# Kernel tuning notes

Hardware: AMD Instinct MI355X
Metric: run time of the kernel (lower is better)

The kernel has to match this reference:

```python
import jax, jax.numpy as jnp
import numpy as np

D_MODEL = 768
HEADS = 12
D_K = D_MODEL // HEADS
NEG = -1e9


def setup_inputs() -> dict:
    key = jax.random.key(0)
    ks = jax.random.split(key, 7)
    B, S, D = 4, 2048, D_MODEL
    scale = 1.0 / np.sqrt(D)
    q = jax.random.normal(ks[0], (B, S, D), dtype=jnp.float32)
    k = jax.random.normal(ks[1], (B, S, D), dtype=jnp.float32)
    v = jax.random.normal(ks[2], (B, S, D), dtype=jnp.float32)
    # causal mask, broadcastable over batch and heads; mask==0 -> -1e9
    mask = jnp.tril(jnp.ones((1, 1, S, S), dtype=jnp.int32))
    W_q = jax.random.normal(ks[3], (D, D), dtype=jnp.float32) * scale
    W_k = jax.random.normal(ks[4], (D, D), dtype=jnp.float32) * scale
    W_v = jax.random.normal(ks[5], (D, D), dtype=jnp.float32) * scale
    W_o = jax.random.normal(ks[6], (D, D), dtype=jnp.float32) * scale
    return {"q": q, "k": k, "v": v, "mask": mask,
            "W_q": W_q, "W_k": W_k, "W_v": W_v, "W_o": W_o}


def reference(q, k, v, mask, W_q, W_k, W_v, W_o):
    B, S, D = q.shape
    # nn.Linear(bias=False): y = x @ W.T
    query = (q @ W_q.T).reshape(B, S, HEADS, D_K).transpose(0, 2, 1, 3)  # [B,H,S,dk]
    key_ = (k @ W_k.T).reshape(B, S, HEADS, D_K).transpose(0, 2, 1, 3)
    value = (v @ W_v.T).reshape(B, S, HEADS, D_K).transpose(0, 2, 1, 3)
    scores = jnp.einsum('bhqd,bhkd->bhqk', query, key_) / jnp.sqrt(
        jnp.asarray(D_K, dtype=query.dtype))
    scores = jnp.where(mask == 0, jnp.asarray(NEG, dtype=scores.dtype), scores)
    attn = jax.nn.softmax(scores, axis=-1)
    # dropout rate = 0.0 (inference / eval mode): identity
    x = jnp.einsum('bhqk,bhkd->bhqd', attn, value)  # [B,H,S,dk]
    x = x.transpose(0, 2, 1, 3).reshape(B, S, D)
    return x @ W_o.T
```

## Files before the change

kernel.cpp:

```cpp
#include <hip/hip_runtime.h>


typedef _Float16 f16x8 __attribute__((ext_vector_type(8)));
typedef _Float16 f16x4 __attribute__((ext_vector_type(4)));
typedef float floatx4 __attribute__((ext_vector_type(4)));
typedef float floatx16 __attribute__((ext_vector_type(16)));

#define MFMA16(a, b, c) __builtin_amdgcn_mfma_f32_16x16x32_f16((a), (b), (c), 0, 0, 0)
#define MFMA32(a, b, c) __builtin_amdgcn_mfma_f32_32x32x16_f16((a), (b), (c), 0, 0, 0)

static constexpr int B_ = 4;
static constexpr int S_ = 2048;
static constexpr int D_ = 768;
static constexpr int H_ = 12;
static constexpr int DK = 64;

__device__ __forceinline__ f16x8 cvt8(float4 a, float4 b) {
  f16x8 h;
  h[0] = (_Float16)a.x; h[1] = (_Float16)a.y;
  h[2] = (_Float16)a.z; h[3] = (_Float16)a.w;
  h[4] = (_Float16)b.x; h[5] = (_Float16)b.y;
  h[6] = (_Float16)b.z; h[7] = (_Float16)b.w;
  return h;
}

__device__ __forceinline__ void dma16(const _Float16* g, _Float16* l) {
  __builtin_amdgcn_global_load_lds(
      (const __attribute__((address_space(1))) unsigned int*)g,
      (__attribute__((address_space(3))) unsigned int*)l, 16, 0, 0);
}

struct CvtArgs {
  const float* src[7];
  _Float16* dst[7];
  int end[7];
  int nseg;
};

__global__ __launch_bounds__(256) void cvt_f32_f16(CvtArgs a) {
  int b = blockIdx.x;
  int s = 0;
  while (s < a.nseg - 1 && b >= a.end[s]) ++s;
  int local = b - (s ? a.end[s - 1] : 0);
  const int tid = threadIdx.x;
  const float4* p = (const float4*)(a.src[s] + (size_t)local * 2048) + tid * 2;
  float4 x0 = p[0], x1 = p[1];
  *(f16x8*)(a.dst[s] + (size_t)local * 2048 + tid * 8) = cvt8(x0, x1);
}

static constexpr int PAN = 128 * 32;

struct QkvPtrs {
  const void* a[3];
  const void* w[3];
};

template <int MODE, bool SCALE>
__device__ __forceinline__ void gemm_core64(const _Float16* __restrict__ A,
                                            const _Float16* __restrict__ Bm,
                                            void* __restrict__ Cv,
                                            _Float16* As, _Float16* Bs,
                                            int m0, int n0, int N, int K) {
  const int tid = threadIdx.x;
  const int wave = tid >> 6, lane = tid & 63;
  const int l15 = lane & 15, quad = lane >> 4;
  const int wm = (wave >> 1) * 64, wn = (wave & 1) * 64;
  const int lr = lane >> 2;
  const int lc = (lane & 3) * 8;
  const int wb = wave * 16;

  floatx4 acc[4][4] = {};

  for (int k0 = 0; k0 < K; k0 += 64) {
    {
      const _Float16* g = A + (size_t)(m0 + wb + lr) * K + k0 + lc;
      dma16(g, As + wb * 32);
      dma16(g + 32, As + PAN + wb * 32);
      const _Float16* g2 = g + (size_t)64 * K;
      dma16(g2, As + (64 + wb) * 32);
      dma16(g2 + 32, As + PAN + (64 + wb) * 32);
    }
    {
      const _Float16* g = Bm + (size_t)(n0 + wb + lr) * K + k0 + lc;
      dma16(g, Bs + wb * 32);
      dma16(g + 32, Bs + PAN + wb * 32);
      const _Float16* g2 = g + (size_t)64 * K;
      dma16(g2, Bs + (64 + wb) * 32);
      dma16(g2 + 32, Bs + PAN + (64 + wb) * 32);
    }
    __syncthreads();

#pragma unroll
    for (int p = 0; p < 2; ++p) {
      f16x8 af[4], bf[4];
#pragma unroll
      for (int t = 0; t < 4; ++t)
        af[t] = *(const f16x8*)(As + p * PAN + (wm + t * 16 + l15) * 32 +
                                quad * 8);
#pragma unroll
      for (int t = 0; t < 4; ++t)
        bf[t] = *(const f16x8*)(Bs + p * PAN + (wn + t * 16 + l15) * 32 +
                                quad * 8);
#pragma unroll
      for (int mt = 0; mt < 4; ++mt)
#pragma unroll
        for (int nt = 0; nt < 4; ++nt)
          acc[mt][nt] = MFMA16(af[mt], bf[nt], acc[mt][nt]);
    }
    __syncthreads();
  }

  if constexpr (MODE == 2) {
#pragma unroll
    for (int mt = 0; mt < 4; ++mt)
#pragma unroll
      for (int nt = 0; nt < 4; ++nt) {
        int row = m0 + wm + mt * 16 + quad * 4;
        int col = n0 + wn + nt * 16 + l15;
        int b = row >> 11, s = row & 2047;
        int h = col >> 6, d = col & 63;
        f16x4 v4;
#pragma unroll
        for (int r = 0; r < 4; ++r) v4[r] = (_Float16)acc[mt][nt][r];
        *(f16x4*)((_Float16*)Cv + ((size_t)(b * H_ + h) * DK + d) * S_ + s) =
            v4;
      }
  } else {
#pragma unroll
    for (int mt = 0; mt < 4; ++mt)
#pragma unroll
      for (int nt = 0; nt < 4; ++nt)
#pragma unroll
        for (int r = 0; r < 4; ++r) {
          int row = m0 + wm + mt * 16 + quad * 4 + r;
          int col = n0 + wn + nt * 16 + l15;
          float val = acc[mt][nt][r];
          if constexpr (SCALE) val *= 0.125f;
          if constexpr (MODE == 0) {
            ((float*)Cv)[(size_t)row * N + col] = val;
          } else {
            int b = row >> 11, s = row & 2047;
            int h = col >> 6, d = col & 63;
            ((_Float16*)Cv)[((size_t)(b * H_ + h) * S_ + s) * DK + d] =
                (_Float16)val;
          }
        }
  }
}

__global__ __launch_bounds__(256) void qkv_gemm64(QkvPtrs P, _Float16* Qh,
                                                  _Float16* Kh, _Float16* Vt) {
  __shared__ _Float16 As[2 * PAN];
  __shared__ _Float16 Bs[2 * PAN];
  const int linear =
      blockIdx.x + gridDim.x * (blockIdx.y + gridDim.y * blockIdx.z);
  const int xcd = linear & 7;
  const int idx = linear >> 3;
  const int z = idx / 48;
  const int r = idx % 48;
  const int mp = xcd * 8 + (r / 6);
  const int n = r % 6;
  const int m0 = mp * 128, n0 = n * 128;
  if (z == 0) {
    gemm_core64<1, true>((const _Float16*)P.a[0], (const _Float16*)P.w[0], Qh,
                         As, Bs, m0, n0, D_, D_);
  } else if (z == 1) {
    gemm_core64<1, false>((const _Float16*)P.a[1], (const _Float16*)P.w[1], Kh,
                          As, Bs, m0, n0, D_, D_);
  } else {
    gemm_core64<2, false>((const _Float16*)P.a[2], (const _Float16*)P.w[2], Vt,
                          As, Bs, m0, n0, D_, D_);
  }
}

static constexpr int PAN_A = 64 * 32;
static constexpr int PAN_B = 128 * 32;

__global__ __launch_bounds__(256) void gemm_o64(const _Float16* __restrict__ A,
                                                const _Float16* __restrict__ W,
                                                float* __restrict__ C) {
  __shared__ _Float16 As[2 * PAN_A];
  __shared__ _Float16 Bs[2 * PAN_B];
  constexpr int K = 768, N = 768;

  const int linear = blockIdx.x + gridDim.x * blockIdx.y;
  const int xcd = linear & 7;
  const int idx = linear >> 3;
  const int mp = xcd * 16 + idx / 6;
  const int n = idx % 6;
  const int m0 = mp * 64, n0 = n * 128;

  const int tid = threadIdx.x;
  const int wave = tid >> 6, lane = tid & 63;
  const int l15 = lane & 15, quad = lane >> 4;
  const int wm = (wave >> 1) * 32, wn = (wave & 1) * 64;
  const int lr = lane >> 2, lc = (lane & 3) * 8;

  floatx4 acc[2][4] = {};

  for (int k0 = 0; k0 < K; k0 += 64) {
#pragma unroll
    for (int p = 0; p < 2; ++p) {
      const _Float16* g =
          A + (size_t)(m0 + wave * 16 + lr) * K + k0 + p * 32 + lc;
      dma16(g, As + p * PAN_A + wave * 16 * 32);
    }
#pragma unroll
    for (int p = 0; p < 2; ++p)
#pragma unroll
      for (int q = 0; q < 2; ++q) {
        const _Float16* g =
            W + (size_t)(n0 + wave * 32 + q * 16 + lr) * K + k0 + p * 32 + lc;
        dma16(g, Bs + p * PAN_B + (wave * 32 + q * 16) * 32);
      }
    __syncthreads();

#pragma unroll
    for (int p = 0; p < 2; ++p) {
      f16x8 af[2], bf[4];
#pragma unroll
      for (int t = 0; t < 2; ++t)
        af[t] = *(const f16x8*)(As + p * PAN_A + (wm + t * 16 + l15) * 32 +
                                quad * 8);
#pragma unroll
      for (int t = 0; t < 4; ++t)
        bf[t] = *(const f16x8*)(Bs + p * PAN_B + (wn + t * 16 + l15) * 32 +
                                quad * 8);
#pragma unroll
      for (int mt = 0; mt < 2; ++mt)
#pragma unroll
        for (int nt = 0; nt < 4; ++nt)
          acc[mt][nt] = MFMA16(af[mt], bf[nt], acc[mt][nt]);
    }
    __syncthreads();
  }

#pragma unroll
  for (int mt = 0; mt < 2; ++mt)
#pragma unroll
    for (int nt = 0; nt < 4; ++nt)
#pragma unroll
      for (int r = 0; r < 4; ++r) {
        int row = m0 + wm + mt * 16 + quad * 4 + r;
        int col = n0 + wn + nt * 16 + l15;
        C[(size_t)row * N + col] = acc[mt][nt][r];
      }
}

__global__ __launch_bounds__(256, 3) void flash_attn(
    const _Float16* __restrict__ Qh, const _Float16* __restrict__ Kh,
    const _Float16* __restrict__ Vt, _Float16* __restrict__ Oh) {
  __shared__ _Float16 Ks[128 * 72];
  __shared__ _Float16 Vts[64 * 136];
  __shared__ _Float16 Ps[4][32 * 36];

  const int tid = threadIdx.x;
  const int wave = tid >> 6, lane = tid & 63;
  const int l31 = lane & 31, sub = lane >> 5;
  const int rowhalf = wave & 1, keyhalf = wave >> 1;

  const int linear = blockIdx.x + gridDim.x * blockIdx.y;
  const int xcd = linear & 7;
  const int seq = linear >> 3;
  const int bh = xcd * 6 + (seq >> 4);
  const int xp = seq & 15;
  const int b = bh / H_, h = bh % H_;
  const size_t base = (size_t)bh * S_ * DK;
  const size_t basev = (size_t)bh * DK * S_;

  const int srow = tid >> 2;
  const int scol = (tid & 3) * 16;
  const int vcol = (tid & 3) * 32;

  for (int c = 0; c < 2; ++c) {
    const int qt = c ? xp : 31 - xp;
    const int q0 = qt * 64;
    const int nt = qt + 1;
    const int iters = (nt + 1) >> 1;
    const int rbase = q0 + rowhalf * 32;

    f16x8 qf[4];
#pragma unroll
    for (int ks = 0; ks < 4; ++ks)
      qf[ks] = *(const f16x8*)(Qh + base + (size_t)(rbase + l31) * DK +
                               ks * 16 + sub * 8);

    floatx16 o0 = {}, o1 = {};
    float plsum[16] = {};

    f16x8 pk[4], pv[4];
    {
      const _Float16* kp = Kh + base + (size_t)srow * DK + scol;
      pk[0] = *(const f16x8*)kp;
      pk[1] = *(const f16x8*)(kp + 8);
      const _Float16* kp2 = kp + (size_t)64 * DK;
      pk[2] = *(const f16x8*)kp2;
      pk[3] = *(const f16x8*)(kp2 + 8);
      const _Float16* vp = Vt + basev + (size_t)srow * S_ + vcol;
#pragma unroll
      for (int j = 0; j < 4; ++j) pv[j] = *(const f16x8*)(vp + j * 8);
    }

    for (int i = 0; i < iters; ++i) {
      __syncthreads();
      *(f16x8*)(Ks + srow * 72 + scol) = pk[0];
      *(f16x8*)(Ks + srow * 72 + scol + 8) = pk[1];
      *(f16x8*)(Ks + (64 + srow) * 72 + scol) = pk[2];
      *(f16x8*)(Ks + (64 + srow) * 72 + scol + 8) = pk[3];
#pragma unroll
      for (int j = 0; j < 4; ++j)
        *(f16x8*)(Vts + srow * 136 + vcol + j * 8) = pv[j];
      __syncthreads();

      if (i + 1 < iters) {
        const int g0 = (i + 1) * 128;
        const _Float16* kp = Kh + base + (size_t)(g0 + srow) * DK + scol;
        pk[0] = *(const f16x8*)kp;
        pk[1] = *(const f16x8*)(kp + 8);
        const _Float16* kp2 = kp + (size_t)64 * DK;
        pk[2] = *(const f16x8*)kp2;
        pk[3] = *(const f16x8*)(kp2 + 8);
        const _Float16* vp = Vt + basev + (size_t)srow * S_ + g0 + vcol;
#pragma unroll
        for (int j = 0; j < 4; ++j) pv[j] = *(const f16x8*)(vp + j * 8);
      }

      const int kb = i * 128 + keyhalf * 64;
      if (kb > rbase + 31) continue;

      floatx16 s0 = {}, s1 = {};
#pragma unroll
      for (int ks = 0; ks < 4; ++ks) {
        f16x8 kf0 = *(const f16x8*)(Ks + (keyhalf * 64 + l31) * 72 + ks * 16 +
                                    sub * 8);
        f16x8 kf1 = *(const f16x8*)(Ks + (keyhalf * 64 + 32 + l31) * 72 +
                                    ks * 16 + sub * 8);
        s0 = MFMA32(qf[ks], kf0, s0);
        s1 = MFMA32(qf[ks], kf1, s1);
      }

#pragma unroll
      for (int t = 0; t < 2; ++t) {
        floatx16 sv = t ? s1 : s0;
        const int cg = kb + t * 32 + l31;
        const bool nm = (kb + t * 32 + 31 > rbase);
#pragma unroll
        for (int reg = 0; reg < 16; ++reg) {
          float s = sv[reg];
          if (nm) {
            int rg = rbase + (reg & 3) + 8 * (reg >> 2) + 4 * sub;
            if (cg > rg) s = -1e30f;
          }
          float e = __expf(s);
          plsum[reg] += e;
          Ps[wave][((reg & 3) + 8 * (reg >> 2) + 4 * sub) * 36 + l31] =
              (_Float16)e;
        }
        f16x8 pf0 = *(const f16x8*)(Ps[wave] + l31 * 36 + sub * 8);
        f16x8 pf1 = *(const f16x8*)(Ps[wave] + l31 * 36 + 16 + sub * 8);
        const int kk = keyhalf * 64 + t * 32;
        f16x8 va0 = *(const f16x8*)(Vts + l31 * 136 + kk + sub * 8);
        f16x8 va1 = *(const f16x8*)(Vts + l31 * 136 + kk + 16 + sub * 8);
        f16x8 vb0 = *(const f16x8*)(Vts + (32 + l31) * 136 + kk + sub * 8);
        f16x8 vb1 = *(const f16x8*)(Vts + (32 + l31) * 136 + kk + 16 + sub * 8);
        o0 = MFMA32(pf0, va0, o0);
        o0 = MFMA32(pf1, va1, o0);
        o1 = MFMA32(pf0, vb0, o1);
        o1 = MFMA32(pf1, vb1, o1);
      }
    }

#pragma unroll
    for (int reg = 0; reg < 16; ++reg) {
      float l = plsum[reg];
      l += __shfl_xor(l, 1);
      l += __shfl_xor(l, 2);
      l += __shfl_xor(l, 4);
      l += __shfl_xor(l, 8);
      l += __shfl_xor(l, 16);
      plsum[reg] = l;
    }

    float* fb = (float*)Ks;
    float* lb = (float*)Vts;
    __syncthreads();
    if (keyhalf == 1) {
      float* d0 = fb + rowhalf * 2048 + lane * 32;
#pragma unroll
      for (int reg = 0; reg < 16; ++reg) {
        d0[reg] = o0[reg];
        d0[16 + reg] = o1[reg];
      }
      float* dl = lb + rowhalf * 1024 + lane * 16;
#pragma unroll
      for (int reg = 0; reg < 16; ++reg) dl[reg] = plsum[reg];
    }
    __syncthreads();
    if (keyhalf == 0) {
      const float* s0p = fb + rowhalf * 2048 + lane * 32;
      const float* slp = lb + rowhalf * 1024 + lane * 16;
#pragma unroll
      for (int reg = 0; reg < 16; ++reg) {
        float inv = 1.0f / (plsum[reg] + slp[reg]);
        int row = rbase + (reg & 3) + 8 * (reg >> 2) + 4 * sub;
        float v0 = (o0[reg] + s0p[reg]) * inv;
        float v1 = (o1[reg] + s0p[16 + reg]) * inv;
        _Float16* op = Oh + ((size_t)(b * S_ + row)) * D_ + h * DK;
        op[l31] = (_Float16)v0;
        op[32 + l31] = (_Float16)v1;
      }
    }
    __syncthreads();
  }
}

template <int MODE, bool SCALE>
__global__ __launch_bounds__(256) void gemm128(const float* __restrict__ Av,
                                               const float* __restrict__ Bv,
                                               void* __restrict__ Cv, int M,
                                               int N, int K) {
  __shared__ _Float16 As[128 * 40];
  __shared__ _Float16 Bs[128 * 40];

  const int tid = threadIdx.x;
  const int wave = tid >> 6, lane = tid & 63;
  const int l15 = lane & 15, quad = lane >> 4;
  const int wm = (wave >> 1) * 64, wn = (wave & 1) * 64;
  const int m0 = blockIdx.y * 128, n0 = blockIdx.x * 128;
  const int srow = tid >> 1, scol = (tid & 1) * 16;

  floatx4 acc[4][4] = {};

  for (int k0 = 0; k0 < K; k0 += 32) {
    {
      const float4* p =
          (const float4*)(Av + (size_t)(m0 + srow) * K + k0 + scol);
      float4 x0 = p[0], x1 = p[1], x2 = p[2], x3 = p[3];
      *(f16x8*)(As + srow * 40 + scol) = cvt8(x0, x1);
      *(f16x8*)(As + srow * 40 + scol + 8) = cvt8(x2, x3);
    }
    {
      const float4* p =
          (const float4*)(Bv + (size_t)(n0 + srow) * K + k0 + scol);
      float4 x0 = p[0], x1 = p[1], x2 = p[2], x3 = p[3];
      *(f16x8*)(Bs + srow * 40 + scol) = cvt8(x0, x1);
      *(f16x8*)(Bs + srow * 40 + scol + 8) = cvt8(x2, x3);
    }
    __syncthreads();

    f16x8 af[4], bf[4];
#pragma unroll
    for (int t = 0; t < 4; ++t)
      af[t] = *(const f16x8*)(As + (wm + t * 16 + l15) * 40 + quad * 8);
#pragma unroll
    for (int t = 0; t < 4; ++t)
      bf[t] = *(const f16x8*)(Bs + (wn + t * 16 + l15) * 40 + quad * 8);
#pragma unroll
    for (int mt = 0; mt < 4; ++mt)
#pragma unroll
      for (int nt = 0; nt < 4; ++nt)
        acc[mt][nt] = MFMA16(af[mt], bf[nt], acc[mt][nt]);
    __syncthreads();
  }

#pragma unroll
  for (int mt = 0; mt < 4; ++mt)
#pragma unroll
    for (int nt = 0; nt < 4; ++nt)
#pragma unroll
      for (int r = 0; r < 4; ++r) {
        int row = m0 + wm + mt * 16 + quad * 4 + r;
        int col = n0 + wn + nt * 16 + l15;
        float val = acc[mt][nt][r];
        if constexpr (SCALE) val *= 0.125f;
        if constexpr (MODE == 0) {
          ((float*)Cv)[(size_t)row * N + col] = val;
        } else if constexpr (MODE == 1) {
          int b = row >> 11, s = row & 2047;
          int h = col >> 6, d = col & 63;
          ((_Float16*)Cv)[((size_t)(b * H_ + h) * S_ + s) * DK + d] =
              (_Float16)val;
        } else {
          int b = col >> 11, s = col & 2047;
          int h = row >> 6, d = row & 63;
          ((_Float16*)Cv)[((size_t)(b * H_ + h) * DK + d) * S_ + s] =
              (_Float16)val;
        }
      }
}

__global__ __launch_bounds__(256) void gemm_out_f32w(
    const _Float16* __restrict__ A, const float* __restrict__ Bv,
    float* __restrict__ C) {
  __shared__ _Float16 As[128 * 40];
  __shared__ _Float16 Bs[128 * 40];
  constexpr int K = 768, N = 768;

  const int tid = threadIdx.x;
  const int wave = tid >> 6, lane = tid & 63;
  const int l15 = lane & 15, quad = lane >> 4;
  const int wm = (wave >> 1) * 64, wn = (wave & 1) * 64;
  const int m0 = blockIdx.y * 128, n0 = blockIdx.x * 128;
  const int srow = tid >> 1, scol = (tid & 1) * 16;

  floatx4 acc[4][4] = {};

  for (int k0 = 0; k0 < K; k0 += 32) {
    {
      const f16x8* p = (const f16x8*)(A + (size_t)(m0 + srow) * K + k0 + scol);
      *(f16x8*)(As + srow * 40 + scol) = p[0];
      *(f16x8*)(As + srow * 40 + scol + 8) = p[1];
    }
    {
      const float4* p =
          (const float4*)(Bv + (size_t)(n0 + srow) * K + k0 + scol);
      float4 x0 = p[0], x1 = p[1], x2 = p[2], x3 = p[3];
      *(f16x8*)(Bs + srow * 40 + scol) = cvt8(x0, x1);
      *(f16x8*)(Bs + srow * 40 + scol + 8) = cvt8(x2, x3);
    }
    __syncthreads();

    f16x8 af[4], bf[4];
#pragma unroll
    for (int t = 0; t < 4; ++t)
      af[t] = *(const f16x8*)(As + (wm + t * 16 + l15) * 40 + quad * 8);
#pragma unroll
    for (int t = 0; t < 4; ++t)
      bf[t] = *(const f16x8*)(Bs + (wn + t * 16 + l15) * 40 + quad * 8);
#pragma unroll
    for (int mt = 0; mt < 4; ++mt)
#pragma unroll
      for (int nt = 0; nt < 4; ++nt)
        acc[mt][nt] = MFMA16(af[mt], bf[nt], acc[mt][nt]);
    __syncthreads();
  }

#pragma unroll
  for (int mt = 0; mt < 4; ++mt)
#pragma unroll
    for (int nt = 0; nt < 4; ++nt)
#pragma unroll
      for (int r = 0; r < 4; ++r) {
        int row = m0 + wm + mt * 16 + quad * 4 + r;
        int col = n0 + wn + nt * 16 + l15;
        C[(size_t)row * N + col] = acc[mt][nt][r];
      }
}

extern "C" void kernel_launch(void* const* d_in, const int* in_sizes, int n_in,
                              void* d_out, int out_size, void* d_ws,
                              size_t ws_size, hipStream_t stream) {
  const float* q = (const float*)d_in[0];
  const float* k = (const float*)d_in[1];
  const float* v = (const float*)d_in[2];
  const float* Wq = (const float*)d_in[4];
  const float* Wk = (const float*)d_in[5];
  const float* Wv = (const float*)d_in[6];
  const float* Wo = (const float*)d_in[7];
  float* out = (float*)d_out;

  const size_t E = (size_t)B_ * H_ * S_ * DK;
  const size_t EW = (size_t)D_ * D_;
  _Float16* Qh = (_Float16*)d_ws;
  _Float16* Kh = Qh + E;
  _Float16* Vt = Kh + E;
  _Float16* Oh = Vt + E;

  const int M = B_ * S_;
  dim3 blk(256);
  dim3 qg(D_ / 128, M / 128, 3);
  dim3 og(D_ / 128, M / 64);
  dim3 pg(D_ / 128, M / 128);
  dim3 fg(16, B_ * H_);

  const size_t need_full = (7 * E + 4 * EW) * 2;

  if (ws_size >= need_full) {
    _Float16* qf = Oh + E;
    _Float16* kf = qf + E;
    _Float16* vf = kf + E;
    _Float16* wqf = vf + E;
    _Float16* wkf = wqf + EW;
    _Float16* wvf = wkf + EW;
    _Float16* wof = wvf + EW;
    CvtArgs ca;
    ca.src[0] = q;  ca.dst[0] = qf;
    ca.src[1] = k;  ca.dst[1] = kf;
    ca.src[2] = v;  ca.dst[2] = vf;
    ca.src[3] = Wq; ca.dst[3] = wqf;
    ca.src[4] = Wk; ca.dst[4] = wkf;
    ca.src[5] = Wv; ca.dst[5] = wvf;
    ca.src[6] = Wo; ca.dst[6] = wof;
    int ends[7] = {3072, 6144, 9216, 9504, 9792, 10080, 10368};
    for (int i = 0; i < 7; ++i) ca.end[i] = ends[i];
    ca.nseg = 7;
    cvt_f32_f16<<<10368, blk, 0, stream>>>(ca);
    QkvPtrs P;
    P.a[0] = qf; P.a[1] = kf; P.a[2] = vf;
    P.w[0] = wqf; P.w[1] = wkf; P.w[2] = wvf;
    qkv_gemm64<<<qg, blk, 0, stream>>>(P, Qh, Kh, Vt);
    flash_attn<<<fg, blk, 0, stream>>>(Qh, Kh, Vt, Oh);
    gemm_o64<<<og, blk, 0, stream>>>(Oh, wof, out);
  } else {
    gemm128<1, true><<<pg, blk, 0, stream>>>(q, Wq, Qh, M, D_, D_);
    gemm128<1, false><<<pg, blk, 0, stream>>>(k, Wk, Kh, M, D_, D_);
    gemm128<2, false><<<dim3(M / 128, D_ / 128), blk, 0, stream>>>(
        Wv, v, Vt, D_, M, D_);
    flash_attn<<<fg, blk, 0, stream>>>(Qh, Kh, Vt, Oh);
    gemm_out_f32w<<<pg, blk, 0, stream>>>(Oh, Wo, out);
  }
}
```

Measured before the change: 299.7 us.

## Load K/V tiles into LDS via direct global-to-LDS DMA instead of register staging

Replaces the register-prefetched K and V tile loads, previously written to padded LDS, with direct global-to-LDS DMA copies (dma16) into an unpadded, panel-split layout of 32-element rows. The point is to free the VGPRs used for prefetch staging and skip the register round trip through ds_write. In exchange, the software prefetch of the next tile is gone: each iteration now issues loads and waits at the barrier, with no overlap of memory and compute. The unpadded 32-wide rows may also cause LDS bank conflicts on the MFMA operand reads.

After: 274.2 us. -8.5%, faster.

```diff
diff --git a/kernel.cpp b/kernel.cpp
--- a/kernel.cpp
+++ b/kernel.cpp
@@ -250,14 +250,16 @@
 __global__ __launch_bounds__(256, 3) void flash_attn(
     const _Float16* __restrict__ Qh, const _Float16* __restrict__ Kh,
     const _Float16* __restrict__ Vt, _Float16* __restrict__ Oh) {
-  __shared__ _Float16 Ks[128 * 72];
-  __shared__ _Float16 Vts[64 * 136];
+  __shared__ _Float16 Ks[2 * 128 * 32];
+  __shared__ _Float16 Vts[4 * 64 * 32];
   __shared__ _Float16 Ps[4][32 * 36];
 
   const int tid = threadIdx.x;
   const int wave = tid >> 6, lane = tid & 63;
   const int l31 = lane & 31, sub = lane >> 5;
   const int rowhalf = wave & 1, keyhalf = wave >> 1;
+  const int lr = lane >> 2;
+  const int lc = (lane & 3) * 8;
 
   const int linear = blockIdx.x + gridDim.x * blockIdx.y;
   const int xcd = linear & 7;
@@ -268,15 +270,10 @@
   const size_t base = (size_t)bh * S_ * DK;
   const size_t basev = (size_t)bh * DK * S_;
 
-  const int srow = tid >> 2;
-  const int scol = (tid & 3) * 16;
-  const int vcol = (tid & 3) * 32;
-
   for (int c = 0; c < 2; ++c) {
     const int qt = c ? xp : 31 - xp;
     const int q0 = qt * 64;
-    const int nt = qt + 1;
-    const int iters = (nt + 1) >> 1;
+    const int iters = (qt + 2) >> 1;
     const int rbase = q0 + rowhalf * 32;
 
     f16x8 qf[4];
@@ -288,86 +285,74 @@
     floatx16 o0 = {}, o1 = {};
     float plsum[16] = {};
 
-    f16x8 pk[4], pv[4];
-    {
-      const _Float16* kp = Kh + base + (size_t)srow * DK + scol;
-      pk[0] = *(const f16x8*)kp;
-      pk[1] = *(const f16x8*)(kp + 8);
-      const _Float16* kp2 = kp + (size_t)64 * DK;
-      pk[2] = *(const f16x8*)kp2;
-      pk[3] = *(const f16x8*)(kp2 + 8);
-      const _Float16* vp = Vt + basev + (size_t)srow * S_ + vcol;
-#pragma unroll
-      for (int j = 0; j < 4; ++j) pv[j] = *(const f16x8*)(vp + j * 8);
-    }
-
     for (int i = 0; i < iters; ++i) {
+      const int g0 = i * 128;
+#pragma unroll
+      for (int p = 0; p < 2; ++p)
+#pragma unroll
+        for (int qq = 0; qq < 2; ++qq) {
+          const _Float16* g = Kh + base +
+                              (size_t)(g0 + wave * 32 + qq * 16 + lr) * DK +
+                              p * 32 + lc;
+          dma16(g, Ks + p * 4096 + (wave * 32 + qq * 16) * 32);
+        }
+#pragma unroll
+      for (int p = 0; p < 4; ++p) {
+        const _Float16* g =
+            Vt + basev + (size_t)(wave * 16 + lr) * S_ + g0 + p * 32 + lc;
+        dma16(g, Vts + p * 2048 + wave * 16 * 32);
+      }
       __syncthreads();
-      *(f16x8*)(Ks + srow * 72 + scol) = pk[0];
-      *(f16x8*)(Ks + srow * 72 + scol + 8) = pk[1];
-      *(f16x8*)(Ks + (64 + srow) * 72 + scol) = pk[2];
-      *(f16x8*)(Ks + (64 + srow) * 72 + scol + 8) = pk[3];
-#pragma unroll
-      for (int j = 0; j < 4; ++j)
-        *(f16x8*)(Vts + srow * 136 + vcol + j * 8) = pv[j];
+
+      const int kb = g0 + keyhalf * 64;
+      if (kb <= rbase + 31) {
+        floatx16 s0 = {}, s1 = {};
+#pragma unroll
+        for (int ks = 0; ks < 4; ++ks) {
+          const int pp = ks >> 1;
+          const int off = (ks & 1) * 16 + sub * 8;
+          f16x8 kf0 =
+              *(const f16x8*)(Ks + pp * 4096 + (keyhalf * 64 + l31) * 32 + off);
+          f16x8 kf1 = *(const f16x8*)(Ks + pp * 4096 +
+                                      (keyhalf * 64 + 32 + l31) * 32 + off);
+          s0 = MFMA32(qf[ks], kf0, s0);
+          s1 = MFMA32(qf[ks], kf1, s1);
+        }
+
+#pragma unroll
+        for (int t = 0; t < 2; ++t) {
+          floatx16 sv = t ? s1 : s0;
+          const int cg = kb + t * 32 + l31;
+          const bool nm = (kb + t * 32 + 31 > rbase);
+#pragma unroll
+          for (int reg = 0; reg < 16; ++reg) {
+            float s = sv[reg];
+            if (nm) {
+              int rg = rbase + (reg & 3) + 8 * (reg >> 2) + 4 * sub;
+              if (cg > rg) s = -1e30f;
+            }
+            float e = __expf(s);
+            plsum[reg] += e;
+            Ps[wave][((reg & 3) + 8 * (reg >> 2) + 4 * sub) * 36 + l31] =
+                (_Float16)e;
+          }
+          f16x8 pf0 = *(const f16x8*)(Ps[wave] + l31 * 36 + sub * 8);
+          f16x8 pf1 = *(const f16x8*)(Ps[wave] + l31 * 36 + 16 + sub * 8);
+          const int vp = keyhalf * 2 + t;
+          f16x8 va0 = *(const f16x8*)(Vts + vp * 2048 + l31 * 32 + sub * 8);
+          f16x8 va1 =
+              *(const f16x8*)(Vts + vp * 2048 + l31 * 32 + 16 + sub * 8);
+          f16x8 vb0 =
+              *(const f16x8*)(Vts + vp * 2048 + (32 + l31) * 32 + sub * 8);
+          f16x8 vb1 =
+              *(const f16x8*)(Vts + vp * 2048 + (32 + l31) * 32 + 16 + sub * 8);
+          o0 = MFMA32(pf0, va0, o0);
+          o0 = MFMA32(pf1, va1, o0);
+          o1 = MFMA32(pf0, vb0, o1);
+          o1 = MFMA32(pf1, vb1, o1);
+        }
+      }
       __syncthreads();
-
-      if (i + 1 < iters) {
-        const int g0 = (i + 1) * 128;
-        const _Float16* kp = Kh + base + (size_t)(g0 + srow) * DK + scol;
-        pk[0] = *(const f16x8*)kp;
-        pk[1] = *(const f16x8*)(kp + 8);
-        const _Float16* kp2 = kp + (size_t)64 * DK;
-        pk[2] = *(const f16x8*)kp2;
-        pk[3] = *(const f16x8*)(kp2 + 8);
-        const _Float16* vp = Vt + basev + (size_t)srow * S_ + g0 + vcol;
-#pragma unroll
-        for (int j = 0; j < 4; ++j) pv[j] = *(const f16x8*)(vp + j * 8);
-      }
-
-      const int kb = i * 128 + keyhalf * 64;
-      if (kb > rbase + 31) continue;
-
-      floatx16 s0 = {}, s1 = {};
-#pragma unroll
-      for (int ks = 0; ks < 4; ++ks) {
-        f16x8 kf0 = *(const f16x8*)(Ks + (keyhalf * 64 + l31) * 72 + ks * 16 +
-                                    sub * 8);
-        f16x8 kf1 = *(const f16x8*)(Ks + (keyhalf * 64 + 32 + l31) * 72 +
-                                    ks * 16 + sub * 8);
-        s0 = MFMA32(qf[ks], kf0, s0);
-        s1 = MFMA32(qf[ks], kf1, s1);
-      }
-
-#pragma unroll
-      for (int t = 0; t < 2; ++t) {
-        floatx16 sv = t ? s1 : s0;
-        const int cg = kb + t * 32 + l31;
-        const bool nm = (kb + t * 32 + 31 > rbase);
-#pragma unroll
-        for (int reg = 0; reg < 16; ++reg) {
-          float s = sv[reg];
-          if (nm) {
-            int rg = rbase + (reg & 3) + 8 * (reg >> 2) + 4 * sub;
-            if (cg > rg) s = -1e30f;
-          }
-          float e = __expf(s);
-          plsum[reg] += e;
-          Ps[wave][((reg & 3) + 8 * (reg >> 2) + 4 * sub) * 36 + l31] =
-              (_Float16)e;
-        }
-        f16x8 pf0 = *(const f16x8*)(Ps[wave] + l31 * 36 + sub * 8);
-        f16x8 pf1 = *(const f16x8*)(Ps[wave] + l31 * 36 + 16 + sub * 8);
-        const int kk = keyhalf * 64 + t * 32;
-        f16x8 va0 = *(const f16x8*)(Vts + l31 * 136 + kk + sub * 8);
-        f16x8 va1 = *(const f16x8*)(Vts + l31 * 136 + kk + 16 + sub * 8);
-        f16x8 vb0 = *(const f16x8*)(Vts + (32 + l31) * 136 + kk + sub * 8);
-        f16x8 vb1 = *(const f16x8*)(Vts + (32 + l31) * 136 + kk + 16 + sub * 8);
-        o0 = MFMA32(pf0, va0, o0);
-        o0 = MFMA32(pf1, va1, o0);
-        o1 = MFMA32(pf0, vb0, o1);
-        o1 = MFMA32(pf1, vb1, o1);
-      }
     }
 
 #pragma unroll
@@ -383,7 +368,6 @@
 
     float* fb = (float*)Ks;
     float* lb = (float*)Vts;
-    __syncthreads();
     if (keyhalf == 1) {
       float* d0 = fb + rowhalf * 2048 + lane * 32;
 #pragma unroll
```
